# Kernel tuning notes

Hardware: AMD Instinct MI355X
Metric: run time of the kernel (lower is better)

## Reference

```python
import jax, jax.numpy as jnp
import numpy as np

TEMPERATURE = 0.07
SCALE_BY_TEMPERATURE = True
N = 4096
D = 256
N_POS = 32768
CHUNK = 128  # row-chunk size for the cdist to bound the [CHUNK, N, D] temp


def setup_inputs() -> dict:
    key = jax.random.key(0)
    k1, k2, k3 = jax.random.split(key, 3)
    out = jax.random.normal(k1, (N, D), dtype=jnp.float32)
    row = jax.random.randint(k2, (N_POS,), 0, N, dtype=jnp.int32)
    col = jax.random.randint(k3, (N_POS,), 0, N, dtype=jnp.int32)
    return {"out": out, "row": row, "col": col}


def _l1_cdist(x):
    """Pairwise Manhattan distance [N, N], computed in row chunks so the
    [CHUNK, N, D] broadcast temporary stays bounded."""
    n, d = x.shape
    xr = x.reshape(n // CHUNK, CHUNK, d)

    def chunk_dist(xc):  # xc: [CHUNK, D] -> [CHUNK, N]
        return jnp.sum(jnp.abs(xc[:, None, :] - x[None, :, :]), axis=-1)

    return jax.lax.map(chunk_dist, xr).reshape(n, n)


def reference(out, row, col):
    n = out.shape[0]
    sim = -_l1_cdist(out) / TEMPERATURE                      # [N, N]
    logits_max = jax.lax.stop_gradient(jnp.max(sim, axis=1, keepdims=True))
    sim = sim - logits_max
    logits_mask = 1.0 - jnp.eye(n, dtype=sim.dtype)          # zero out self-sims
    denom = jnp.log(jnp.sum(jnp.exp(sim) * logits_mask, axis=1, keepdims=True))
    log_probs = sim - denom                                  # [N, N]
    loss = -jnp.mean(log_probs[row, col])                    # gather positive pairs
    if SCALE_BY_TEMPERATURE:
        loss = loss * TEMPERATURE
    return loss
```

## Files before the change

kernel.cpp:

```cpp
#include <hip/hip_runtime.h>
#include <math.h>

#define N 4096
#define D 256
#define NPOS 32768
#define TEMP 0.07f
#define INVT (1.0f / 0.07f)
#define BIGF 3.0e38f

#define RQ 5.5f
#define QS (255.0f / (2.0f * RQ))
#define DEQ (2.0f * RQ / 255.0f)

#define NT 64
#define NTRI (NT * (NT + 1) / 2)
#define KC 16
#define LP 68

#define WS_PSTAT 0
#define WS_T    (2 * N * NT)
#define WS_ACC  (2 * N * NT + N)
#define WS_CNT  (2 * N * NT + N + 1)
#define WS_XQ   (2 * N * NT + N + 4)

__device__ __forceinline__ void sad_acc(unsigned a, unsigned b, unsigned& c) {
#if __has_builtin(__builtin_amdgcn_sad_u8)
    c = __builtin_amdgcn_sad_u8(a, b, c);
#else
    asm("v_sad_u8 %0, %1, %2, %0" : "+v"(c) : "v"(a), "v"(b));
#endif
}

__device__ __forceinline__ unsigned quant1(float v) {
    const float f = fminf(fmaxf((v + RQ) * QS, 0.0f), 255.0f);
    return (unsigned)__float2uint_rn(f);
}

__global__ __launch_bounds__(256)
void cvt_init_k(const float* __restrict__ x, unsigned* __restrict__ xq,
                float* __restrict__ acc, unsigned* __restrict__ cnt) {
    const int i = blockIdx.x * 256 + threadIdx.x;
    const float4 v = ((const float4*)x)[i];
    const unsigned q = quant1(v.x) | (quant1(v.y) << 8) |
                       (quant1(v.z) << 16) | (quant1(v.w) << 24);
    xq[i] = q;
    if (i == 0) { *acc = 0.0f; *cnt = 0u; }
}

__global__ __launch_bounds__(128, 4)
void dist_tile_k(const unsigned* __restrict__ xq, float2* __restrict__ pstat) {
    const int tt = blockIdx.x;
    const int u_ = (NTRI - 1) - tt;
    int r = (int)((sqrtf((float)(8 * u_ + 1)) - 1.0f) * 0.5f);
    while (r * (r + 1) / 2 > u_) --r;
    while ((r + 1) * (r + 2) / 2 <= u_) ++r;
    const int bm = (NT - 1) - r;
    const int bn = (NT - 1) - (u_ - r * (r + 1) / 2);
    const bool diag = (bm == bn);

    const int tid = threadIdx.x;
    const int lane = tid & 63;
    const int w = tid >> 6;
    const int tx = lane & 7;
    const int ty = lane >> 3;

    __shared__ unsigned As[KC][LP];
    __shared__ unsigned Bs[KC][LP];
    __shared__ float rmin_s[2][64];
    __shared__ float rsum_s[2][64];

    unsigned uacc[2][4][4];
#pragma unroll
    for (int rh = 0; rh < 2; ++rh)
#pragma unroll
        for (int i = 0; i < 4; ++i)
#pragma unroll
            for (int j = 0; j < 4; ++j) uacc[rh][i][j] = 0u;

    const int rowA0 = bm * 64;
    const int rowB0 = bn * 64;

    const int sr = tid >> 2;
    const int su = tid & 3;
    const uint4* gA0 = (const uint4*)xq + (size_t)(rowA0 + sr) * 16 + su;
    const uint4* gA1 = (const uint4*)xq + (size_t)(rowA0 + sr + 32) * 16 + su;
    const uint4* gB0 = (const uint4*)xq + (size_t)(rowB0 + sr) * 16 + su;
    const uint4* gB1 = (const uint4*)xq + (size_t)(rowB0 + sr + 32) * 16 + su;

    const int boff = w * 32 + tx * 4;

    for (int chk = 0; chk < 4; ++chk) {
        const uint4 la0 = gA0[chk * 4];
        const uint4 la1 = gA1[chk * 4];
        const uint4 lb0 = gB0[chk * 4];
        const uint4 lb1 = gB1[chk * 4];
        __syncthreads();
        As[su * 4 + 0][sr] = la0.x; As[su * 4 + 1][sr] = la0.y;
        As[su * 4 + 2][sr] = la0.z; As[su * 4 + 3][sr] = la0.w;
        As[su * 4 + 0][sr + 32] = la1.x; As[su * 4 + 1][sr + 32] = la1.y;
        As[su * 4 + 2][sr + 32] = la1.z; As[su * 4 + 3][sr + 32] = la1.w;
        Bs[su * 4 + 0][sr] = lb0.x; Bs[su * 4 + 1][sr] = lb0.y;
        Bs[su * 4 + 2][sr] = lb0.z; Bs[su * 4 + 3][sr] = lb0.w;
        Bs[su * 4 + 0][sr + 32] = lb1.x; Bs[su * 4 + 1][sr + 32] = lb1.y;
        Bs[su * 4 + 2][sr + 32] = lb1.z; Bs[su * 4 + 3][sr + 32] = lb1.w;
        __syncthreads();

#pragma unroll
        for (int k4 = 0; k4 < KC; ++k4) {
            const uint4 alo = *(const uint4*)&As[k4][ty * 4];
            const uint4 ahi = *(const uint4*)&As[k4][32 + ty * 4];
            const uint4 bw = *(const uint4*)&Bs[k4][boff];
            const unsigned av[2][4] = {{alo.x, alo.y, alo.z, alo.w},
                                       {ahi.x, ahi.y, ahi.z, ahi.w}};
            const unsigned bv[4] = {bw.x, bw.y, bw.z, bw.w};
#pragma unroll
            for (int rh = 0; rh < 2; ++rh)
#pragma unroll
                for (int i = 0; i < 4; ++i)
#pragma unroll
                    for (int j = 0; j < 4; ++j)
                        sad_acc(av[rh][i], bv[j], uacc[rh][i][j]);
        }
    }

    float acc[2][4][4];
#pragma unroll
    for (int rh = 0; rh < 2; ++rh)
#pragma unroll
        for (int i = 0; i < 4; ++i)
#pragma unroll
            for (int j = 0; j < 4; ++j)
                acc[rh][i][j] = (float)uacc[rh][i][j] * DEQ;

    if (diag) {
#pragma unroll
        for (int rh = 0; rh < 2; ++rh)
#pragma unroll
            for (int i = 0; i < 4; ++i)
#pragma unroll
                for (int j = 0; j < 4; ++j)
                    if (rh * 32 + ty * 4 + i == w * 32 + tx * 4 + j)
                        acc[rh][i][j] = BIGF;
    }

#pragma unroll
    for (int rh = 0; rh < 2; ++rh) {
#pragma unroll
        for (int i = 0; i < 4; ++i) {
            float mn = BIGF;
#pragma unroll
            for (int j = 0; j < 4; ++j) mn = fminf(mn, acc[rh][i][j]);
            mn = fminf(mn, __shfl_xor(mn, 1, 64));
            mn = fminf(mn, __shfl_xor(mn, 2, 64));
            mn = fminf(mn, __shfl_xor(mn, 4, 64));
            float s = 0.0f;
#pragma unroll
            for (int j = 0; j < 4; ++j)
                s += __expf((mn - acc[rh][i][j]) * INVT);
            s += __shfl_xor(s, 1, 64);
            s += __shfl_xor(s, 2, 64);
            s += __shfl_xor(s, 4, 64);
            if (tx == 0) {
                rmin_s[w][rh * 32 + ty * 4 + i] = mn;
                rsum_s[w][rh * 32 + ty * 4 + i] = s;
            }
        }
    }

    if (!diag) {
#pragma unroll
        for (int j = 0; j < 4; ++j) {
            float mn = BIGF;
#pragma unroll
            for (int rh = 0; rh < 2; ++rh)
#pragma unroll
                for (int i = 0; i < 4; ++i) mn = fminf(mn, acc[rh][i][j]);
            mn = fminf(mn, __shfl_xor(mn, 8, 64));
            mn = fminf(mn, __shfl_xor(mn, 16, 64));
            mn = fminf(mn, __shfl_xor(mn, 32, 64));
            float s = 0.0f;
#pragma unroll
            for (int rh = 0; rh < 2; ++rh)
#pragma unroll
                for (int i = 0; i < 4; ++i)
                    s += __expf((mn - acc[rh][i][j]) * INVT);
            s += __shfl_xor(s, 8, 64);
            s += __shfl_xor(s, 16, 64);
            s += __shfl_xor(s, 32, 64);
            if (ty == 0)
                pstat[(size_t)(rowB0 + w * 32 + tx * 4 + j) * NT + bm] =
                    make_float2(mn, s);
        }
    }

    __syncthreads();
    if (tid < 64) {
        const float m0 = rmin_s[0][tid], m1 = rmin_s[1][tid];
        const float mn = fminf(m0, m1);
        const float s = rsum_s[0][tid] * __expf((mn - m0) * INVT) +
                        rsum_s[1][tid] * __expf((mn - m1) * INVT);
        pstat[(size_t)(rowA0 + tid) * NT + bn] = make_float2(mn, s);
    }
}

__global__ __launch_bounds__(256)
void row_stats_k(const float2* __restrict__ pstat, float* __restrict__ t) {
    const int r = blockIdx.x * 4 + (threadIdx.x >> 6);
    const int c = threadIdx.x & 63;
    const float2 p = pstat[(size_t)r * NT + c];
    float mn = p.x;
#pragma unroll
    for (int off = 32; off > 0; off >>= 1) mn = fminf(mn, __shfl_xor(mn, off, 64));
    float s = p.y * __expf((mn - p.x) * INVT);
#pragma unroll
    for (int off = 32; off > 0; off >>= 1) s += __shfl_xor(s, off, 64);
    if (c == 0) t[r] = TEMP * __logf(s) - mn;
}

__global__ __launch_bounds__(256)
void pair_fin_k(const float* __restrict__ x, const int* __restrict__ row,
                const int* __restrict__ col, const float* __restrict__ t,
                float* __restrict__ acc, unsigned* __restrict__ cnt,
                float* __restrict__ out) {
    const int lane = threadIdx.x & 63;
    const int wave = threadIdx.x >> 6;
    const int p0 = (blockIdx.x * 4 + wave) * 8;

    int rp[8], cp[8];
#pragma unroll
    for (int i = 0; i < 8; ++i) { rp[i] = row[p0 + i]; cp[i] = col[p0 + i]; }
    float4 a[8], b[8];
#pragma unroll
    for (int i = 0; i < 8; ++i) {
        a[i] = *(const float4*)&x[(size_t)rp[i] * D + lane * 4];
        b[i] = *(const float4*)&x[(size_t)cp[i] * D + lane * 4];
    }
    float wsum = 0.0f;
#pragma unroll
    for (int i = 0; i < 8; ++i) {
        float d = fabsf(a[i].x - b[i].x) + fabsf(a[i].y - b[i].y) +
                  fabsf(a[i].z - b[i].z) + fabsf(a[i].w - b[i].w);
#pragma unroll
        for (int off = 32; off > 0; off >>= 1) d += __shfl_xor(d, off, 64);
        if (lane == 0) wsum += d + t[rp[i]];
    }

    __shared__ float bs[4];
    if (lane == 0) bs[wave] = wsum;
    __syncthreads();
    if (threadIdx.x == 0) {
        const float tot = bs[0] + bs[1] + bs[2] + bs[3];
        atomicAdd(acc, tot);
        __threadfence();
        const unsigned tk = atomicAdd(cnt, 1u);
        if (tk == (unsigned)(gridDim.x - 1)) {
            const float v = atomicAdd(acc, 0.0f);
            out[0] = v * (1.0f / (float)NPOS);
        }
    }
}

extern "C" void kernel_launch(void* const* d_in, const int* in_sizes, int n_in,
                              void* d_out, int out_size, void* d_ws, size_t ws_size,
                              hipStream_t stream) {
    const float* x = (const float*)d_in[0];
    const int* row = (const int*)d_in[1];
    const int* col = (const int*)d_in[2];
    float* ws = (float*)d_ws;
    float* out = (float*)d_out;
    unsigned* xq = (unsigned*)(ws + WS_XQ);
    float* acc = ws + WS_ACC;
    unsigned* cnt = (unsigned*)(ws + WS_CNT);

    cvt_init_k<<<(N * D / 4) / 256, 256, 0, stream>>>(x, xq, acc, cnt);

    dist_tile_k<<<NTRI, 128, 0, stream>>>(xq, (float2*)(ws + WS_PSTAT));

    row_stats_k<<<N / 4, 256, 0, stream>>>((const float2*)(ws + WS_PSTAT), ws + WS_T);

    pair_fin_k<<<NPOS / 32, 256, 0, stream>>>(x, row, col, ws + WS_T, acc, cnt, out);
}
```

Before: 126.0 us.

## Use single-wave 8x8 register tiles with register prefetch in SAD distance kernel

The distance tile kernel now runs one 64-lane wave per 64x64 tile, and each lane accumulates an 8x8 block instead of two 4x4 blocks. This raises arithmetic per LDS read and removes the cross-wave shared-memory merge of row statistics. The next K chunk is prefetched from global memory into registers while the current chunk is computed. In exchange, register pressure rises (64 accumulators plus prefetch buffers), and there are fewer threads per block, which may lower occupancy and latency hiding.

After: 357.9 us. 2.84x slower.

```diff
diff --git a/kernel.cpp b/kernel.cpp
--- a/kernel.cpp
+++ b/kernel.cpp
@@ -47,7 +47,7 @@
     if (i == 0) { *acc = 0.0f; *cnt = 0u; }
 }
 
-__global__ __launch_bounds__(128, 4)
+__global__ __launch_bounds__(64, 2)
 void dist_tile_k(const unsigned* __restrict__ xq, float2* __restrict__ pstat) {
     const int tt = blockIdx.x;
     const int u_ = (NTRI - 1) - tt;
@@ -58,148 +58,136 @@
     const int bn = (NT - 1) - (u_ - r * (r + 1) / 2);
     const bool diag = (bm == bn);
 
-    const int tid = threadIdx.x;
-    const int lane = tid & 63;
-    const int w = tid >> 6;
+    const int lane = threadIdx.x;
     const int tx = lane & 7;
     const int ty = lane >> 3;
 
     __shared__ unsigned As[KC][LP];
     __shared__ unsigned Bs[KC][LP];
-    __shared__ float rmin_s[2][64];
-    __shared__ float rsum_s[2][64];
-
-    unsigned uacc[2][4][4];
-#pragma unroll
-    for (int rh = 0; rh < 2; ++rh)
-#pragma unroll
-        for (int i = 0; i < 4; ++i)
-#pragma unroll
-            for (int j = 0; j < 4; ++j) uacc[rh][i][j] = 0u;
+
+    unsigned uacc[8][8];
+#pragma unroll
+    for (int i = 0; i < 8; ++i)
+#pragma unroll
+        for (int j = 0; j < 8; ++j) uacc[i][j] = 0u;
 
     const int rowA0 = bm * 64;
     const int rowB0 = bn * 64;
 
-    const int sr = tid >> 2;
-    const int su = tid & 3;
-    const uint4* gA0 = (const uint4*)xq + (size_t)(rowA0 + sr) * 16 + su;
-    const uint4* gA1 = (const uint4*)xq + (size_t)(rowA0 + sr + 32) * 16 + su;
-    const uint4* gB0 = (const uint4*)xq + (size_t)(rowB0 + sr) * 16 + su;
-    const uint4* gB1 = (const uint4*)xq + (size_t)(rowB0 + sr + 32) * 16 + su;
-
-    const int boff = w * 32 + tx * 4;
-
+    const int sr = lane >> 2;
+    const int su = lane & 3;
+    const uint4* gA = (const uint4*)xq + (size_t)(rowA0 + sr) * 16 + su;
+    const uint4* gB = (const uint4*)xq + (size_t)(rowB0 + sr) * 16 + su;
+
+    uint4 la[4], lb[4];
+#pragma unroll
+    for (int k = 0; k < 4; ++k) {
+        la[k] = gA[k * 256];
+        lb[k] = gB[k * 256];
+    }
+
+#pragma unroll 1
     for (int chk = 0; chk < 4; ++chk) {
-        const uint4 la0 = gA0[chk * 4];
-        const uint4 la1 = gA1[chk * 4];
-        const uint4 lb0 = gB0[chk * 4];
-        const uint4 lb1 = gB1[chk * 4];
         __syncthreads();
-        As[su * 4 + 0][sr] = la0.x; As[su * 4 + 1][sr] = la0.y;
-        As[su * 4 + 2][sr] = la0.z; As[su * 4 + 3][sr] = la0.w;
-        As[su * 4 + 0][sr + 32] = la1.x; As[su * 4 + 1][sr + 32] = la1.y;
-        As[su * 4 + 2][sr + 32] = la1.z; As[su * 4 + 3][sr + 32] = la1.w;
-        Bs[su * 4 + 0][sr] = lb0.x; Bs[su * 4 + 1][sr] = lb0.y;
-        Bs[su * 4 + 2][sr] = lb0.z; Bs[su * 4 + 3][sr] = lb0.w;
-        Bs[su * 4 + 0][sr + 32] = lb1.x; Bs[su * 4 + 1][sr + 32] = lb1.y;
-        Bs[su * 4 + 2][sr + 32] = lb1.z; Bs[su * 4 + 3][sr + 32] = lb1.w;
+#pragma unroll
+        for (int k = 0; k < 4; ++k) {
+            As[su * 4 + 0][sr + 16 * k] = la[k].x;
+            As[su * 4 + 1][sr + 16 * k] = la[k].y;
+            As[su * 4 + 2][sr + 16 * k] = la[k].z;
+            As[su * 4 + 3][sr + 16 * k] = la[k].w;
+            Bs[su * 4 + 0][sr + 16 * k] = lb[k].x;
+            Bs[su * 4 + 1][sr + 16 * k] = lb[k].y;
+            Bs[su * 4 + 2][sr + 16 * k] = lb[k].z;
+            Bs[su * 4 + 3][sr + 16 * k] = lb[k].w;
+        }
+        uint4 na[4], nb[4];
+        if (chk < 3) {
+#pragma unroll
+            for (int k = 0; k < 4; ++k) {
+                na[k] = gA[k * 256 + (chk + 1) * 4];
+                nb[k] = gB[k * 256 + (chk + 1) * 4];
+            }
+        }
         __syncthreads();
 
 #pragma unroll
         for (int k4 = 0; k4 < KC; ++k4) {
-            const uint4 alo = *(const uint4*)&As[k4][ty * 4];
-            const uint4 ahi = *(const uint4*)&As[k4][32 + ty * 4];
-            const uint4 bw = *(const uint4*)&Bs[k4][boff];
-            const unsigned av[2][4] = {{alo.x, alo.y, alo.z, alo.w},
-                                       {ahi.x, ahi.y, ahi.z, ahi.w}};
-            const unsigned bv[4] = {bw.x, bw.y, bw.z, bw.w};
-#pragma unroll
-            for (int rh = 0; rh < 2; ++rh)
-#pragma unroll
-                for (int i = 0; i < 4; ++i)
-#pragma unroll
-                    for (int j = 0; j < 4; ++j)
-                        sad_acc(av[rh][i], bv[j], uacc[rh][i][j]);
-        }
-    }
-
-    float acc[2][4][4];
-#pragma unroll
-    for (int rh = 0; rh < 2; ++rh)
-#pragma unroll
-        for (int i = 0; i < 4; ++i)
-#pragma unroll
-            for (int j = 0; j < 4; ++j)
-                acc[rh][i][j] = (float)uacc[rh][i][j] * DEQ;
+            const uint4 a0 = *(const uint4*)&As[k4][ty * 8];
+            const uint4 a1 = *(const uint4*)&As[k4][ty * 8 + 4];
+            const uint4 b0 = *(const uint4*)&Bs[k4][tx * 8];
+            const uint4 b1 = *(const uint4*)&Bs[k4][tx * 8 + 4];
+            const unsigned av[8] = {a0.x, a0.y, a0.z, a0.w,
+                                    a1.x, a1.y, a1.z, a1.w};
+            const unsigned bv[8] = {b0.x, b0.y, b0.z, b0.w,
+                                    b1.x, b1.y, b1.z, b1.w};
+#pragma unroll
+            for (int i = 0; i < 8; ++i)
+#pragma unroll
+                for (int j = 0; j < 8; ++j)
+                    sad_acc(av[i], bv[j], uacc[i][j]);
+        }
+
+        if (chk < 3) {
+#pragma unroll
+            for (int k = 0; k < 4; ++k) { la[k] = na[k]; lb[k] = nb[k]; }
+        }
+    }
+
+    float acc[8][8];
+#pragma unroll
+    for (int i = 0; i < 8; ++i)
+#pragma unroll
+        for (int j = 0; j < 8; ++j)
+            acc[i][j] = (float)uacc[i][j] * DEQ;
 
     if (diag) {
 #pragma unroll
-        for (int rh = 0; rh < 2; ++rh)
-#pragma unroll
-            for (int i = 0; i < 4; ++i)
-#pragma unroll
-                for (int j = 0; j < 4; ++j)
-                    if (rh * 32 + ty * 4 + i == w * 32 + tx * 4 + j)
-                        acc[rh][i][j] = BIGF;
-    }
-
-#pragma unroll
-    for (int rh = 0; rh < 2; ++rh) {
-#pragma unroll
-        for (int i = 0; i < 4; ++i) {
+        for (int i = 0; i < 8; ++i)
+#pragma unroll
+            for (int j = 0; j < 8; ++j)
+                if (ty * 8 + i == tx * 8 + j)
+                    acc[i][j] = BIGF;
+    }
+
+#pragma unroll
+    for (int i = 0; i < 8; ++i) {
+        float mn = BIGF;
+#pragma unroll
+        for (int j = 0; j < 8; ++j) mn = fminf(mn, acc[i][j]);
+        mn = fminf(mn, __shfl_xor(mn, 1, 64));
+        mn = fminf(mn, __shfl_xor(mn, 2, 64));
+        mn = fminf(mn, __shfl_xor(mn, 4, 64));
+        float s = 0.0f;
+#pragma unroll
+        for (int j = 0; j < 8; ++j)
+            s += __expf((mn - acc[i][j]) * INVT);
+        s += __shfl_xor(s, 1, 64);
+        s += __shfl_xor(s, 2, 64);
+        s += __shfl_xor(s, 4, 64);
+        if (tx == 0)
+            pstat[(size_t)(rowA0 + ty * 8 + i) * NT + bn] = make_float2(mn, s);
+    }
+
+    if (!diag) {
+#pragma unroll
+        for (int j = 0; j < 8; ++j) {
             float mn = BIGF;
 #pragma unroll
-            for (int j = 0; j < 4; ++j) mn = fminf(mn, acc[rh][i][j]);
-            mn = fminf(mn, __shfl_xor(mn, 1, 64));
-            mn = fminf(mn, __shfl_xor(mn, 2, 64));
-            mn = fminf(mn, __shfl_xor(mn, 4, 64));
-            float s = 0.0f;
-#pragma unroll
-            for (int j = 0; j < 4; ++j)
-                s += __expf((mn - acc[rh][i][j]) * INVT);
-            s += __shfl_xor(s, 1, 64);
-            s += __shfl_xor(s, 2, 64);
-            s += __shfl_xor(s, 4, 64);
-            if (tx == 0) {
-                rmin_s[w][rh * 32 + ty * 4 + i] = mn;
-                rsum_s[w][rh * 32 + ty * 4 + i] = s;
-            }
-        }
-    }
-
-    if (!diag) {
-#pragma unroll
-        for (int j = 0; j < 4; ++j) {
-            float mn = BIGF;
-#pragma unroll
-            for (int rh = 0; rh < 2; ++rh)
-#pragma unroll
-                for (int i = 0; i < 4; ++i) mn = fminf(mn, acc[rh][i][j]);
+            for (int i = 0; i < 8; ++i) mn = fminf(mn, acc[i][j]);
             mn = fminf(mn, __shfl_xor(mn, 8, 64));
             mn = fminf(mn, __shfl_xor(mn, 16, 64));
             mn = fminf(mn, __shfl_xor(mn, 32, 64));
             float s = 0.0f;
 #pragma unroll
-            for (int rh = 0; rh < 2; ++rh)
-#pragma unroll
-                for (int i = 0; i < 4; ++i)
-                    s += __expf((mn - acc[rh][i][j]) * INVT);
+            for (int i = 0; i < 8; ++i)
+                s += __expf((mn - acc[i][j]) * INVT);
             s += __shfl_xor(s, 8, 64);
             s += __shfl_xor(s, 16, 64);
             s += __shfl_xor(s, 32, 64);
             if (ty == 0)
-                pstat[(size_t)(rowB0 + w * 32 + tx * 4 + j) * NT + bm] =
+                pstat[(size_t)(rowB0 + tx * 8 + j) * NT + bm] =
                     make_float2(mn, s);
         }
-    }
-
-    __syncthreads();
-    if (tid < 64) {
-        const float m0 = rmin_s[0][tid], m1 = rmin_s[1][tid];
-        const float mn = fminf(m0, m1);
-        const float s = rsum_s[0][tid] * __expf((mn - m0) * INVT) +
-                        rsum_s[1][tid] * __expf((mn - m1) * INVT);
-        pstat[(size_t)(rowA0 + tid) * NT + bn] = make_float2(mn, s);
     }
 }
 
@@ -274,7 +262,7 @@
 
     cvt_init_k<<<(N * D / 4) / 256, 256, 0, stream>>>(x, xq, acc, cnt);
 
-    dist_tile_k<<<NTRI, 128, 0, stream>>>(xq, (float2*)(ws + WS_PSTAT));
+    dist_tile_k<<<NTRI, 64, 0, stream>>>(xq, (float2*)(ws + WS_PSTAT));
 
     row_stats_k<<<N / 4, 256, 0, stream>>>((const float2*)(ws + WS_PSTAT), ws + WS_T);
 
```
